# Optimization experiments

Hardware: AMD Instinct MI355X
Metric: run time of the kernel (lower is better)

## Reference

```python
import jax, jax.numpy as jnp
import numpy as np

EMBED = 1024
HEADS = 16
HEAD_DIM = EMBED // HEADS


def setup_inputs() -> dict:
    key = jax.random.key(0)
    ks = jax.random.split(key, 12)
    B, S = 2, 2048
    inp = {
        'v': jax.random.normal(ks[0], (B, S, EMBED), jnp.float32),
        'k': jax.random.normal(ks[1], (B, S, EMBED), jnp.float32),
        'q': jax.random.normal(ks[2], (B, S, EMBED), jnp.float32),
        'mask': jnp.ones((B, 1, S, S), dtype=bool),
        'Wv': jax.random.normal(ks[3], (EMBED, EMBED), jnp.float32) * 0.02,
        'bv': jax.random.normal(ks[4], (EMBED,), jnp.float32) * 0.02,
        'Wk': jax.random.normal(ks[5], (EMBED, EMBED), jnp.float32) * 0.02,
        'bk': jax.random.normal(ks[6], (EMBED,), jnp.float32) * 0.02,
        'Wq': jax.random.normal(ks[7], (EMBED, EMBED), jnp.float32) * 0.02,
        'bq': jax.random.normal(ks[8], (EMBED,), jnp.float32) * 0.02,
        'Wo': jax.random.normal(ks[9], (EMBED, EMBED), jnp.float32) * 0.02,
        'bo': jax.random.normal(ks[10], (EMBED,), jnp.float32) * 0.02,
    }
    return inp


def reference(v, k, q, mask, Wv, bv, Wk, bk, Wq, bq, Wo, bo):
    N, q_len, _ = q.shape
    k_len = k.shape[1]
    # linear projections (torch Linear: x @ W.T + b)
    vh = (v @ Wv.T + bv).reshape(N, -1, HEADS, HEAD_DIM)
    kh = (k @ Wk.T + bk).reshape(N, k_len, HEADS, HEAD_DIM)
    qh = (q @ Wq.T + bq).reshape(N, q_len, HEADS, HEAD_DIM)
    # scores [N, H, q, k]
    energy = jnp.einsum('nqhd,nkhd->nhqk', qh, kh)
    # NOTE: original masks BEFORE dividing by sqrt(embed_size)
    energy = jnp.where(mask, energy, jnp.float32(-1e20))
    attention = jax.nn.softmax(energy / jnp.sqrt(jnp.float32(EMBED)), axis=3)
    out = jnp.einsum('nhqk,nkhd->nqhd', attention, vh).reshape(N, q_len, EMBED)
    return out @ Wo.T + bo
```

## Files before the change

### kernel.cpp

```cpp
#include <hip/hip_runtime.h>
#include <cstdint>
#include <cstddef>


typedef uint16_t u16;
typedef uint32_t u32;
typedef unsigned long long u64;
using bf16x8 = __attribute__((ext_vector_type(8))) __bf16;
using bf16x2 = __attribute__((ext_vector_type(2))) __bf16;
using f32x4  = __attribute__((ext_vector_type(4))) float;
using f32x16 = __attribute__((ext_vector_type(16))) float;
using u16x8  = __attribute__((ext_vector_type(8))) uint16_t;
using u16x4  = __attribute__((ext_vector_type(4))) uint16_t;
using u32x4  = __attribute__((ext_vector_type(4))) uint32_t;

#define S_LEN 2048
#define EMB   1024
#define NHEAD 16
#define HDIM  64
#define BATCH 2
#define MROWS (BATCH * S_LEN)
#define NBITW (BATCH * S_LEN * (S_LEN / 64))

__device__ __forceinline__ u16 f2bf(float f) {
  uint32_t u = __float_as_uint(f);
  u += 0x7FFFu + ((u >> 16) & 1u);
  return (u16)(u >> 16);
}

__device__ __forceinline__ float fexp2(float x) {
#if __has_builtin(__builtin_amdgcn_exp2f)
  return __builtin_amdgcn_exp2f(x);
#else
  return exp2f(x);
#endif
}

__device__ __forceinline__ u32 packbf(float a, float b) {
  bf16x2 v = { (__bf16)a, (__bf16)b };
  return __builtin_bit_cast(u32, v);
}

__device__ __forceinline__ void plswap(u32& a, u32& b) {
  asm volatile("v_permlane32_swap_b32 %0, %1" : "+v"(a), "+v"(b));
}

__device__ __forceinline__ float xhalf_sum(float x) {
  u32 a = __builtin_bit_cast(u32, x), b;
  asm volatile("v_mov_b32 %0, %1" : "=v"(b) : "v"(a));
  asm volatile("v_permlane32_swap_b32 %0, %1" : "+v"(a), "+v"(b));
  return __builtin_bit_cast(float, a) + __builtin_bit_cast(float, b);
}

__device__ __forceinline__ float tree16(const f32x16& v) {
  float t0 = v[0] + v[1], t1 = v[2] + v[3], t2 = v[4] + v[5], t3 = v[6] + v[7];
  float t4 = v[8] + v[9], t5 = v[10] + v[11], t6 = v[12] + v[13], t7 = v[14] + v[15];
  float u0 = t0 + t1, u1 = t2 + t3, u2 = t4 + t5, u3 = t6 + t7;
  return (u0 + u1) + (u2 + u3);
}

__device__ __forceinline__ void async16(void* lds, const void* g) {
  __builtin_amdgcn_global_load_lds(
      (const __attribute__((address_space(1))) void*)g,
      (__attribute__((address_space(3))) void*)lds, 16, 0, 0);
}

__global__ __launch_bounds__(256) void mask_compact(const uint32_t* __restrict__ m,
                                                    u64* __restrict__ bits) {
  const int i = blockIdx.x * 256 + threadIdx.x;
  if (i >= NBITW) return;
  const bool bytew = (m[0] == 0x01010101u);
  u64 b = 0;
  if (bytew) {
    const uint32_t* src = m + (size_t)i * 16;
#pragma unroll
    for (int w = 0; w < 16; ++w) {
      const uint32_t v = src[w];
#pragma unroll
      for (int j = 0; j < 4; ++j)
        b |= (u64)(((v >> (8 * j)) & 0xFFu) != 0u) << (w * 4 + j);
    }
  } else {
    const uint32_t* src = m + (size_t)i * 64;
#pragma unroll
    for (int j = 0; j < 64; ++j) b |= (u64)(src[j] != 0u) << j;
  }
  bits[i] = b;
}

struct ConvArgs {
  const float* src[7];
  u16* dst[7];
  int n4[7];
};

__global__ __launch_bounds__(256) void convert_bf16(ConvArgs a) {
  const int j = blockIdx.y;
  const float4* s = (const float4*)a.src[j];
  u16* d = a.dst[j];
  const int n4 = a.n4[j];
  for (int i = blockIdx.x * 256 + threadIdx.x; i < n4; i += gridDim.x * 256) {
    float4 v = s[i];
    u16x4 o = { f2bf(v.x), f2bf(v.y), f2bf(v.z), f2bf(v.w) };
    *(u16x4*)(d + (size_t)i * 4) = o;
  }
}

template <int BM, int FM, typename OutT>
__device__ __forceinline__ void gemm_body_bk64(const u16* __restrict__ A,
                                               const u16* __restrict__ W,
                                               const float* __restrict__ bias,
                                               OutT* __restrict__ C, float scale,
                                               int m0, int n0) {
  constexpr int K = 1024, N = 1024;
  __shared__ alignas(16) u16 As[BM * 64];
  __shared__ alignas(16) u16 Bs[128 * 64];
  const int t = threadIdx.x;
  const int wave = t >> 6, lane = t & 63;
  const int wr = wave >> 1, wc = wave & 1;
  f32x4 acc[FM][4] = {};
  const int f = lane >> 3;
  const int soff = ((lane & 7) ^ f) * 8;
  const int srowp = wave * 8 + f;
  const int fr = lane & 15;
  const int q4 = lane >> 4;

  for (int kt = 0; kt < K; kt += 64) {
#pragma unroll
    for (int i = 0; i < BM / 32; ++i)
      async16(As + i * 2048 + wave * 512,
              A + (size_t)(m0 + i * 32 + srowp) * K + kt + soff);
#pragma unroll
    for (int i = 0; i < 4; ++i)
      async16(Bs + i * 2048 + wave * 512,
              W + (size_t)(n0 + i * 32 + srowp) * K + kt + soff);
    __syncthreads();
#pragma unroll
    for (int kk = 0; kk < 2; ++kk) {
      bf16x8 af[FM], bfr[4];
#pragma unroll
      for (int i = 0; i < FM; ++i) {
        const int row = wr * (FM * 16) + i * 16 + fr;
        af[i] = *(const bf16x8*)((const char*)As + row * 128 +
                                 (((q4 + kk * 4) ^ (row & 7)) << 4));
      }
#pragma unroll
      for (int i = 0; i < 4; ++i) {
        const int row = wc * 64 + i * 16 + fr;
        bfr[i] = *(const bf16x8*)((const char*)Bs + row * 128 +
                                  (((q4 + kk * 4) ^ (row & 7)) << 4));
      }
#pragma unroll
      for (int mi = 0; mi < FM; ++mi)
#pragma unroll
        for (int ni = 0; ni < 4; ++ni)
          acc[mi][ni] = __builtin_amdgcn_mfma_f32_16x16x32_bf16(
              af[mi], bfr[ni], acc[mi][ni], 0, 0, 0);
    }
    __syncthreads();
  }
  const int r0 = (lane >> 4) * 4;
#pragma unroll
  for (int mi = 0; mi < FM; ++mi) {
    const int rowb = m0 + wr * (FM * 16) + mi * 16 + r0;
#pragma unroll
    for (int ni = 0; ni < 4; ++ni) {
      const int col = n0 + wc * 64 + ni * 16 + fr;
      const float bv = bias[col];
#pragma unroll
      for (int r = 0; r < 4; ++r) {
        const float v = (acc[mi][ni][r] + bv) * scale;
        if constexpr (sizeof(OutT) == 2)
          C[(size_t)(rowb + r) * N + col] = f2bf(v);
        else
          C[(size_t)(rowb + r) * N + col] = v;
      }
    }
  }
}

struct ProjArgs {
  const u16* A[3];
  const u16* W[3];
  const float* bias[3];
  u16* C[3];
  float scale[3];
};

__global__ __launch_bounds__(256) void gemm_proj3(ProjArgs p) {
  const int lin = blockIdx.x + 8 * blockIdx.y + 256 * blockIdx.z;
  const int logical = (lin & 7) * 96 + (lin >> 3);
  const int z = logical >> 8;
  const int rem = logical & 255;
  const int n0 = (rem & 7) * 128, m0 = (rem >> 3) * 128;
  gemm_body_bk64<128, 4, u16>(p.A[z], p.W[z], p.bias[z], p.C[z], p.scale[z],
                              m0, n0);
}

__global__ __launch_bounds__(256) void gemm_out(const u16* __restrict__ A,
                                                const u16* __restrict__ W,
                                                const float* __restrict__ bias,
                                                float* __restrict__ C) {
  const int lin = blockIdx.x + 8 * blockIdx.y;
  const int logical = (lin & 7) * 64 + (lin >> 3);
  const int m0 = (logical >> 3) * 64, n0 = (logical & 7) * 128;
  gemm_body_bk64<64, 2, float>(A, W, bias, C, 1.0f, m0, n0);
}

__global__ __launch_bounds__(256, 2) void attn_fa(const u16* __restrict__ Qh,
                                                  const u16* __restrict__ Kh,
                                                  const u16* __restrict__ Vh,
                                                  const u64* __restrict__ mbits,
                                                  u16* __restrict__ O) {
  __shared__ alignas(16) u16 Kt[2][64 * 64];
  __shared__ alignas(16) u16 Vt[2][64 * 64];
  const int t = threadIdx.x, wave = t >> 6, lane = t & 63;
  const int lin = blockIdx.x + 16 * blockIdx.y;
  const int logical = (lin & 7) * 64 + (lin >> 3);
  const int wbx = logical & 15;
  const int wbh = logical >> 4;
  const int b = wbh >> 4, h = wbh & 15;
  const int ql = lane & 31;
  const int hi = lane >> 5;
  const int qrow = wbx * 128 + wave * 32 + ql;

  const u16* qbase = Qh + (size_t)(b * S_LEN + qrow) * EMB + h * HDIM + hi * 8;
  bf16x8 qf[4];
#pragma unroll
  for (int dk = 0; dk < 4; ++dk)
    qf[dk] = *(const bf16x8*)(qbase + dk * 16);

  const int srow = t >> 3;
  const int schunk = t & 7;
  const int fk0 = (srow + (srow >> 3)) & 7;
  const int fk1 = (srow + 32 + ((srow + 32) >> 3)) & 7;
  const u16* kbase = Kh + (size_t)(b * S_LEN) * EMB + h * HDIM;
  const u16* vbase = Vh + (size_t)(b * S_LEN) * EMB + h * HDIM;
  const int vdg = t & 7, vkp = t >> 3;
  const int vd0 = vdg * 8, vk0 = vkp * 2;
  const int vg_hi = (vkp >> 2) & 7, vg_lo = (vkp & 3) * 4;

  u16x8 va, vb;
  {
    async16(&Kt[0][0] + wave * 512,
            kbase + (size_t)srow * EMB + ((schunk ^ fk0) * 8));
    async16(&Kt[0][0] + 2048 + wave * 512,
            kbase + (size_t)(srow + 32) * EMB + ((schunk ^ fk1) * 8));
    const u16* vs = vbase + (size_t)vk0 * EMB + vd0;
    va = *(const u16x8*)vs;
    vb = *(const u16x8*)(vs + EMB);
  }
#pragma unroll
  for (int j = 0; j < 8; ++j) {
    const int d = vd0 + j;
    const int fd = (d + (d >> 3)) & 7;
    const u32 val = (u32)va[j] | ((u32)vb[j] << 16);
    *(u32*)((char*)&Vt[0][0] + (d * 128 + ((vg_hi ^ fd) << 4) + vg_lo)) = val;
  }
  __syncthreads();

  f32x16 o[2] = {};
  float lloc = 0.f;
  const u64* mword = mbits + (size_t)(b * S_LEN + qrow) * 32;

  for (int kt = 0; kt < 32; ++kt) {
    const int cur = kt & 1, nxt = cur ^ 1;
    if (kt < 31) {
      const int kvn = (kt + 1) * 64;
      async16(&Kt[nxt][0] + wave * 512,
              kbase + (size_t)(kvn + srow) * EMB + ((schunk ^ fk0) * 8));
      async16(&Kt[nxt][0] + 2048 + wave * 512,
              kbase + (size_t)(kvn + srow + 32) * EMB + ((schunk ^ fk1) * 8));
      const u16* vs = vbase + (size_t)(kvn + vk0) * EMB + vd0;
      va = *(const u16x8*)vs;
      vb = *(const u16x8*)(vs + EMB);
    }

    f32x16 s[2] = {};
    __builtin_amdgcn_s_setprio(1);
#pragma unroll
    for (int kb = 0; kb < 2; ++kb) {
      const int key = kb * 32 + ql;
      const int fkk = (key + (key >> 3)) & 7;
      const char* kRow = (const char*)&Kt[cur][0] + key * 128;
#pragma unroll
      for (int dk = 0; dk < 4; ++dk) {
        const bf16x8 kf =
            *(const bf16x8*)(kRow + (((dk * 2 + hi) ^ fkk) << 4));
        s[kb] = __builtin_amdgcn_mfma_f32_32x32x16_bf16(kf, qf[dk], s[kb], 0, 0, 0);
      }
    }
    __builtin_amdgcn_s_setprio(0);

    const u64 mw = mword[kt];
    if (!__all((int)(mw == ~0ull))) {
#pragma unroll
      for (int kb = 0; kb < 2; ++kb)
#pragma unroll
        for (int r = 0; r < 16; ++r) {
          const int key = 32 * kb + (r & 3) + 8 * (r >> 2) + 4 * hi;
          if (!((mw >> key) & 1ull)) s[kb][r] = -1.0e20f;
        }
    }

#pragma unroll
    for (int kb = 0; kb < 2; ++kb)
#pragma unroll
      for (int r = 0; r < 16; ++r) s[kb][r] = fexp2(s[kb][r]);
    lloc += tree16(s[0]) + tree16(s[1]);

    bf16x8 pf[4];
#pragma unroll
    for (int kb = 0; kb < 2; ++kb) {
      u32 w0 = packbf(s[kb][0], s[kb][1]);
      u32 w1 = packbf(s[kb][2], s[kb][3]);
      u32 w2 = packbf(s[kb][4], s[kb][5]);
      u32 w3 = packbf(s[kb][6], s[kb][7]);
      u32 w4 = packbf(s[kb][8], s[kb][9]);
      u32 w5 = packbf(s[kb][10], s[kb][11]);
      u32 w6 = packbf(s[kb][12], s[kb][13]);
      u32 w7 = packbf(s[kb][14], s[kb][15]);
      plswap(w0, w2);
      plswap(w1, w3);
      plswap(w4, w6);
      plswap(w5, w7);
      const u32x4 lo4 = {w0, w1, w2, w3};
      const u32x4 hi4 = {w4, w5, w6, w7};
      pf[kb * 2 + 0] = __builtin_bit_cast(bf16x8, lo4);
      pf[kb * 2 + 1] = __builtin_bit_cast(bf16x8, hi4);
    }

    __builtin_amdgcn_s_setprio(1);
#pragma unroll
    for (int dB = 0; dB < 2; ++dB) {
      const int d = dB * 32 + ql;
      const int fd = (d + (d >> 3)) & 7;
      const char* vRow = (const char*)&Vt[cur][0] + d * 128;
#pragma unroll
      for (int ks = 0; ks < 4; ++ks) {
        const bf16x8 vf =
            *(const bf16x8*)(vRow + (((ks * 2 + hi) ^ fd) << 4));
        o[dB] = __builtin_amdgcn_mfma_f32_32x32x16_bf16(vf, pf[ks], o[dB], 0, 0, 0);
      }
    }
    __builtin_amdgcn_s_setprio(0);

    if (kt < 31) {
#pragma unroll
      for (int j = 0; j < 8; ++j) {
        const int d = vd0 + j;
        const int fd = (d + (d >> 3)) & 7;
        const u32 val = (u32)va[j] | ((u32)vb[j] << 16);
        *(u32*)((char*)&Vt[nxt][0] + (d * 128 + ((vg_hi ^ fd) << 4) + vg_lo)) = val;
      }
    }
    __syncthreads();
  }

  const float inv = 1.0f / xhalf_sum(lloc);
  u16* ob = O + (size_t)(b * S_LEN + qrow) * EMB + h * HDIM;
#pragma unroll
  for (int dB = 0; dB < 2; ++dB)
#pragma unroll
    for (int rr = 0; rr < 4; ++rr) {
      u16x4 st;
#pragma unroll
      for (int m = 0; m < 4; ++m) st[m] = f2bf(o[dB][rr * 4 + m] * inv);
      *(u16x4*)(ob + dB * 32 + rr * 8 + hi * 4) = st;
    }
}

extern "C" void kernel_launch(void* const* d_in, const int* in_sizes, int n_in,
                              void* d_out, int out_size, void* d_ws, size_t ws_size,
                              hipStream_t stream) {
  const float* v_in = (const float*)d_in[0];
  const float* k_in = (const float*)d_in[1];
  const float* q_in = (const float*)d_in[2];
  const uint32_t* mask = (const uint32_t*)d_in[3];
  const float* Wv = (const float*)d_in[4];
  const float* bv = (const float*)d_in[5];
  const float* Wk = (const float*)d_in[6];
  const float* bk = (const float*)d_in[7];
  const float* Wq = (const float*)d_in[8];
  const float* bq = (const float*)d_in[9];
  const float* Wo = (const float*)d_in[10];
  const float* bo = (const float*)d_in[11];

  char* ws = (char*)d_ws;
  const size_t SZX = (size_t)MROWS * EMB * 2;
  const size_t SZW = (size_t)EMB * EMB * 2;
  u16* qh  = (u16*)(ws);
  u16* kh  = (u16*)(ws + SZX);
  u16* vh  = (u16*)(ws + 2 * SZX);
  u16* Obf = (u16*)(ws + 3 * SZX);
  u16* Wqb = (u16*)(ws + 4 * SZX);
  u16* Wkb = (u16*)(ws + 4 * SZX + SZW);
  u16* Wvb = (u16*)(ws + 4 * SZX + 2 * SZW);
  u16* Wob = (u16*)(ws + 4 * SZX + 3 * SZW);
  u16* qbf = (u16*)(ws + 4 * SZX + 4 * SZW);
  u16* kbf = (u16*)(ws + 5 * SZX + 4 * SZW);
  u16* vbf = (u16*)(ws + 6 * SZX + 4 * SZW);
  u64* mbits = (u64*)(ws + 7 * SZX + 4 * SZW);

  mask_compact<<<dim3(NBITW / 256), 256, 0, stream>>>(mask, mbits);

  ConvArgs ca;
  ca.src[0] = q_in; ca.dst[0] = qbf; ca.n4[0] = MROWS * EMB / 4;
  ca.src[1] = k_in; ca.dst[1] = kbf; ca.n4[1] = MROWS * EMB / 4;
  ca.src[2] = v_in; ca.dst[2] = vbf; ca.n4[2] = MROWS * EMB / 4;
  ca.src[3] = Wq;   ca.dst[3] = Wqb; ca.n4[3] = EMB * EMB / 4;
  ca.src[4] = Wk;   ca.dst[4] = Wkb; ca.n4[4] = EMB * EMB / 4;
  ca.src[5] = Wv;   ca.dst[5] = Wvb; ca.n4[5] = EMB * EMB / 4;
  ca.src[6] = Wo;   ca.dst[6] = Wob; ca.n4[6] = EMB * EMB / 4;
  convert_bf16<<<dim3(256, 7), 256, 0, stream>>>(ca);

  ProjArgs pa;
  const float qscale = 1.4426950408889634f / 32.0f;
  pa.A[0] = qbf; pa.W[0] = Wqb; pa.bias[0] = bq; pa.C[0] = qh; pa.scale[0] = qscale;
  pa.A[1] = kbf; pa.W[1] = Wkb; pa.bias[1] = bk; pa.C[1] = kh; pa.scale[1] = 1.0f;
  pa.A[2] = vbf; pa.W[2] = Wvb; pa.bias[2] = bv; pa.C[2] = vh; pa.scale[2] = 1.0f;
  gemm_proj3<<<dim3(8, 32, 3), 256, 0, stream>>>(pa);

  attn_fa<<<dim3(16, 32), 256, 0, stream>>>(qh, kh, vh, mbits, Obf);

  gemm_out<<<dim3(8, 64), 256, 0, stream>>>(Obf, Wob, bo, (float*)d_out);
}
```

Before: 130.2 us.

## Split attention over two key halves and merge partials in a combine kernel

The flash-attention kernel now takes a z grid dimension. Each block handles half of the key sequence and writes an unnormalized bf16 partial output plus its per-row softmax denominator. A new combine kernel adds the two partials, divides by the summed denominators and writes the normalized bf16 output. This doubles the block count to improve load balance, at the cost of an extra launch, extra global traffic for the partial buffers and one more bf16 rounding step.

```diff
diff --git a/kernel.cpp b/kernel.cpp
--- a/kernel.cpp
+++ b/kernel.cpp
@@ -26,6 +26,9 @@
   uint32_t u = __float_as_uint(f);
   u += 0x7FFFu + ((u >> 16) & 1u);
   return (u16)(u >> 16);
+}
+__device__ __forceinline__ float bf2f(u16 x) {
+  return __uint_as_float((u32)x << 16);
 }
 
 __device__ __forceinline__ float fexp2(float x) {
@@ -211,10 +214,14 @@
                                                   const u16* __restrict__ Kh,
                                                   const u16* __restrict__ Vh,
                                                   const u64* __restrict__ mbits,
-                                                  u16* __restrict__ O) {
+                                                  u16* __restrict__ P0,
+                                                  u16* __restrict__ P1,
+                                                  float* __restrict__ L0,
+                                                  float* __restrict__ L1) {
   __shared__ alignas(16) u16 Kt[2][64 * 64];
   __shared__ alignas(16) u16 Vt[2][64 * 64];
   const int t = threadIdx.x, wave = t >> 6, lane = t & 63;
+  const int z = blockIdx.z;
   const int lin = blockIdx.x + 16 * blockIdx.y;
   const int logical = (lin & 7) * 64 + (lin >> 3);
   const int wbx = logical & 15;
@@ -234,8 +241,8 @@
   const int schunk = t & 7;
   const int fk0 = (srow + (srow >> 3)) & 7;
   const int fk1 = (srow + 32 + ((srow + 32) >> 3)) & 7;
-  const u16* kbase = Kh + (size_t)(b * S_LEN) * EMB + h * HDIM;
-  const u16* vbase = Vh + (size_t)(b * S_LEN) * EMB + h * HDIM;
+  const u16* kbase = Kh + (size_t)(b * S_LEN + z * 1024) * EMB + h * HDIM;
+  const u16* vbase = Vh + (size_t)(b * S_LEN + z * 1024) * EMB + h * HDIM;
   const int vdg = t & 7, vkp = t >> 3;
   const int vd0 = vdg * 8, vk0 = vkp * 2;
   const int vg_hi = (vkp >> 2) & 7, vg_lo = (vkp & 3) * 4;
@@ -261,11 +268,11 @@
 
   f32x16 o[2] = {};
   float lloc = 0.f;
-  const u64* mword = mbits + (size_t)(b * S_LEN + qrow) * 32;
-
-  for (int kt = 0; kt < 32; ++kt) {
+  const u64* mword = mbits + (size_t)(b * S_LEN + qrow) * 32 + z * 16;
+
+  for (int kt = 0; kt < 16; ++kt) {
     const int cur = kt & 1, nxt = cur ^ 1;
-    if (kt < 31) {
+    if (kt < 15) {
       const int kvn = (kt + 1) * 64;
       async16(&Kt[nxt][0] + wave * 512,
               kbase + (size_t)(kvn + srow) * EMB + ((schunk ^ fk0) * 8));
@@ -345,7 +352,7 @@
     }
     __builtin_amdgcn_s_setprio(0);
 
-    if (kt < 31) {
+    if (kt < 15) {
 #pragma unroll
       for (int j = 0; j < 8; ++j) {
         const int d = vd0 + j;
@@ -357,17 +364,40 @@
     __syncthreads();
   }
 
-  const float inv = 1.0f / xhalf_sum(lloc);
-  u16* ob = O + (size_t)(b * S_LEN + qrow) * EMB + h * HDIM;
+  const float lsum = xhalf_sum(lloc);
+  u16* Pz = z ? P1 : P0;
+  float* Lz = z ? L1 : L0;
+  u16* pb = Pz + (size_t)(b * S_LEN + qrow) * EMB + h * HDIM;
 #pragma unroll
   for (int dB = 0; dB < 2; ++dB)
 #pragma unroll
     for (int rr = 0; rr < 4; ++rr) {
       u16x4 st;
 #pragma unroll
-      for (int m = 0; m < 4; ++m) st[m] = f2bf(o[dB][rr * 4 + m] * inv);
-      *(u16x4*)(ob + dB * 32 + rr * 8 + hi * 4) = st;
-    }
+      for (int m = 0; m < 4; ++m) st[m] = f2bf(o[dB][rr * 4 + m]);
+      *(u16x4*)(pb + dB * 32 + rr * 8 + hi * 4) = st;
+    }
+  if (hi == 0)
+    Lz[(size_t)(b * S_LEN + qrow) * NHEAD + h] = lsum;
+}
+
+__global__ __launch_bounds__(256) void attn_combine(const u16* __restrict__ P0,
+                                                    const u16* __restrict__ P1,
+                                                    const float* __restrict__ L0,
+                                                    const float* __restrict__ L1,
+                                                    u16* __restrict__ O) {
+  const int i = blockIdx.x * 256 + threadIdx.x;
+  const int row = i >> 7;
+  const int h = (i & 127) >> 3;
+  const int li = row * NHEAD + h;
+  const float inv = 1.0f / (L0[li] + L1[li]);
+  const u16x8 a = *(const u16x8*)(P0 + (size_t)i * 8);
+  const u16x8 b = *(const u16x8*)(P1 + (size_t)i * 8);
+  u16x8 r;
+#pragma unroll
+  for (int j = 0; j < 8; ++j)
+    r[j] = f2bf((bf2f(a[j]) + bf2f(b[j])) * inv);
+  *(u16x8*)(O + (size_t)i * 8) = r;
 }
 
 extern "C" void kernel_launch(void* const* d_in, const int* in_sizes, int n_in,
@@ -401,6 +431,10 @@
   u16* kbf = (u16*)(ws + 5 * SZX + 4 * SZW);
   u16* vbf = (u16*)(ws + 6 * SZX + 4 * SZW);
   u64* mbits = (u64*)(ws + 7 * SZX + 4 * SZW);
+  u16* Pp0 = qbf;
+  u16* Pp1 = kbf;
+  float* Lp0 = (float*)vbf;
+  float* Lp1 = (float*)(ws + 6 * SZX + 4 * SZW + (1 << 20));
 
   mask_compact<<<dim3(NBITW / 256), 256, 0, stream>>>(mask, mbits);
 
@@ -421,7 +455,11 @@
   pa.A[2] = vbf; pa.W[2] = Wvb; pa.bias[2] = bv; pa.C[2] = vh; pa.scale[2] = 1.0f;
   gemm_proj3<<<dim3(8, 32, 3), 256, 0, stream>>>(pa);
 
-  attn_fa<<<dim3(16, 32), 256, 0, stream>>>(qh, kh, vh, mbits, Obf);
+  attn_fa<<<dim3(16, 32, 2), 256, 0, stream>>>(qh, kh, vh, mbits,
+                                               Pp0, Pp1, Lp0, Lp1);
+
+  attn_combine<<<dim3(MROWS * EMB / 8 / 256), 256, 0, stream>>>(
+      Pp0, Pp1, Lp0, Lp1, Obf);
 
   gemm_out<<<dim3(8, 64), 256, 0, stream>>>(Obf, Wob, bo, (float*)d_out);
 }
```

New measurement: 139.2 us. +6.9%, slower.
